# Kernel tuning notes

Measured on AMD Instinct MI355X. Metric: run time of the kernel, lower is better.

## Reference

```python
import jax, jax.numpy as jnp
import numpy as np

DIM = 1024
HEADS = 16
BLK = 129
DK = 64
DV = 64
B = 4
N = BLK * 32  # 4128


def setup_inputs() -> dict:
    key = jax.random.key(0)
    ks = jax.random.split(key, 6)
    inner_k = HEADS * DK
    inner_v = HEADS * DV
    s = 1.0 / np.sqrt(DIM)
    x = jax.random.normal(ks[0], (B, N, DIM), dtype=jnp.float32)
    Wq = jax.random.normal(ks[1], (inner_k, DIM), dtype=jnp.float32) * s
    Wk = jax.random.normal(ks[2], (inner_k, DIM), dtype=jnp.float32) * s
    Wv = jax.random.normal(ks[3], (inner_v, DIM), dtype=jnp.float32) * s
    Wo = jax.random.normal(ks[4], (DIM, inner_v), dtype=jnp.float32) * (1.0 / np.sqrt(inner_v))
    bo = jax.random.normal(ks[5], (DIM,), dtype=jnp.float32) * 0.01
    return {"x": x, "Wq": Wq, "Wk": Wk, "Wv": Wv, "Wo": Wo, "bo": bo}


def reference(x, Wq, Wk, Wv, Wo, bo):
    Bsz, Nlen, D = x.shape
    nb = Nlen // BLK
    scale = 1.0 / np.sqrt(DK)
    # projections (Linear without bias: x @ W.T)
    q = (x @ Wq.T).reshape(Bsz, nb, BLK, HEADS, DK)
    k = (x @ Wk.T).reshape(Bsz, nb, BLK, HEADS, DK)
    v = (x @ Wv.T).reshape(Bsz, nb, BLK, HEADS, DV)
    # block-local attention: each block attends within itself
    scores = jnp.einsum('bnqhd,bnkhd->bnhqk', q, k) * scale  # [B,nb,H,BLK,BLK]
    attn = jax.nn.softmax(scores, axis=-1)
    out_blk = jnp.einsum('bnhqk,bnkhd->bnhqd', attn, v)  # [B,nb,H,BLK,DV]
    # global attention among the first token of each block
    qg = q[:, :, 0]  # [B,nb,H,DK]
    kg = k[:, :, 0]
    vg = v[:, :, 0]
    sg = jnp.einsum('bqhd,bkhd->bhqk', qg, kg) * scale  # [B,H,nb,nb]
    ag = jax.nn.softmax(sg, axis=-1)
    out_g = jnp.einsum('bhqk,bkhd->bqhd', ag, vg)  # [B,nb,H,DV]
    # add global output onto position 0 of each block
    out_blk = out_blk.at[:, :, :, 0, :].add(out_g.transpose(0, 1, 2, 3).swapaxes(2, 2))  # out_g already [B,nb,H,DV]
    # reassemble to [B,N,H*DV]
    out = out_blk.transpose(0, 1, 3, 2, 4).reshape(Bsz, Nlen, HEADS * DV)
    return out @ Wo.T + bo
```

## Files before the change

### kernel.cpp

```cpp
#include <hip/hip_runtime.h>

typedef unsigned short u16;
typedef __attribute__((ext_vector_type(8))) __bf16 bf16x8;
typedef __attribute__((ext_vector_type(4))) float f32x4;
typedef __attribute__((ext_vector_type(8))) u16 u16x8;
typedef __attribute__((ext_vector_type(4))) u16 u16x4;

#define DIMSZ 1024
#define HEADS 16
#define BLKSZ 129
#define NBLK 32
#define NTOK (BLKSZ * NBLK)
#define BATCH 4
#define MROWS (BATCH * NTOK)

#define MFMA __builtin_amdgcn_mfma_f32_16x16x32_bf16

#define SSTR 152
#define KSTR 72

#define NKT 32

__device__ __forceinline__ float bf2f(u16 u) {
  return __uint_as_float(((unsigned)u) << 16);
}
__device__ __forceinline__ u16 f2bf(float f) {
  unsigned u = __float_as_uint(f);
  u += 0x7FFFu + ((u >> 16) & 1u);
  return (u16)(u >> 16);
}

#define GLD16(ldsp, gp) __builtin_amdgcn_global_load_lds( \
    (const __attribute__((address_space(1))) void*)(gp),   \
    (__attribute__((address_space(3))) void*)(ldsp), 16, 0, 0)

__global__ __launch_bounds__(256) void cast_f32_bf16(
    const float* __restrict__ in, u16* __restrict__ out, int n)
{
  int i = (blockIdx.x * 256 + threadIdx.x) * 4;
  if (i < n) {
    float4 f = *(const float4*)(in + i);
    u16x4 o = { f2bf(f.x), f2bf(f.y), f2bf(f.z), f2bf(f.w) };
    *(u16x4*)(out + i) = o;
  }
}

__device__ __forceinline__ int xcd_swz(int bid, int nwg) {
  const int xcd = bid & 7, l = bid >> 3;
  const int q = nwg >> 3, r = nwg & 7;
  return (xcd < r ? xcd * (q + 1) : r * (q + 1) + (xcd - r) * q) + l;
}

__device__ __forceinline__ void stage3(u16* slot, const u16* gA,
                                       const u16* gB, int tid) {
  GLD16(slot + tid * 8, gA);
  GLD16(slot + 4096 + tid * 8, gB);
  GLD16(slot + 8192 + tid * 8, gB + 128 * DIMSZ);
}

__device__ __forceinline__ void gemm_pipe(
    const u16* __restrict__ A, const u16* __restrict__ Bm,
    int m0, int n0, int tid, u16 (*sm)[12288], f32x4 (*acc)[4])
{
  const int lane = tid & 63, w = tid >> 6;
  const int qd = lane >> 4, l15 = lane & 15;
  const int wm = (w >> 2) * 64, wn = (w & 3) * 64;

  const u16* gA = A + (size_t)(m0 + (tid >> 2)) * DIMSZ + (tid & 3) * 8;
  const u16* gB = Bm + (size_t)(n0 + (tid >> 2)) * DIMSZ + (tid & 3) * 8;

  stage3(sm[0], gA, gB, tid);
  stage3(sm[1], gA + 32, gB + 32, tid);
  asm volatile("s_waitcnt vmcnt(3)" ::: "memory");
  __builtin_amdgcn_s_barrier();
  __builtin_amdgcn_sched_barrier(0);

#pragma unroll 4
  for (int t = 0; t < NKT; ++t) {
    if (t + 2 < NKT)
      stage3(sm[(t + 2) & 3], gA + (t + 2) * 32, gB + (t + 2) * 32, tid);

    const u16* slot = sm[t & 3];
    bf16x8 af[4], bv[4];
#pragma unroll
    for (int mi = 0; mi < 4; ++mi)
      af[mi] = *(const bf16x8*)&slot[(wm + mi * 16 + l15) * 32 + qd * 8];
#pragma unroll
    for (int ni = 0; ni < 4; ++ni)
      bv[ni] = *(const bf16x8*)&slot[4096 + (wn + ni * 16 + l15) * 32 + qd * 8];

    __builtin_amdgcn_s_setprio(1);
#pragma unroll
    for (int mi = 0; mi < 4; ++mi)
#pragma unroll
      for (int ni = 0; ni < 4; ++ni)
        acc[mi][ni] = MFMA(af[mi], bv[ni], acc[mi][ni], 0, 0, 0);
    __builtin_amdgcn_s_setprio(0);

    __builtin_amdgcn_sched_barrier(0);
    if (t + 2 < NKT) {
      asm volatile("s_waitcnt vmcnt(3)" ::: "memory");
    } else {
      asm volatile("s_waitcnt vmcnt(0)" ::: "memory");
    }
    __builtin_amdgcn_s_barrier();
    __builtin_amdgcn_sched_barrier(0);
  }
}

__global__ __launch_bounds__(512, 2) void gemm_qkv(
    const u16* __restrict__ A, const u16* __restrict__ B,
    u16* __restrict__ Cq, u16* __restrict__ Ck, u16* __restrict__ Cv)
{
  __shared__ u16 sm[4][12288];
  const int tid = threadIdx.x;
  f32x4 acc[4][4];
#pragma unroll
  for (int mi = 0; mi < 4; ++mi)
#pragma unroll
    for (int ni = 0; ni < 4; ++ni)
      acc[mi][ni] = (f32x4){0.f, 0.f, 0.f, 0.f};

  const int wg = xcd_swz(blockIdx.x, (MROWS / 128) * 12);
  const int nt = wg % 12, mt = wg / 12;
  const int m0 = mt * 128, n0 = nt * 256;

  gemm_pipe(A, B, m0, n0, tid, sm, acc);

  u16* C = nt < 4 ? Cq : (nt < 8 ? Ck : Cv);
  const int c0 = (nt & 3) * 256;
  const int lane = tid & 63, w = tid >> 6;
  const int qd = lane >> 4, l15 = lane & 15;
  const int wm = (w >> 2) * 64, wn = (w & 3) * 64;
#pragma unroll
  for (int mi = 0; mi < 4; ++mi)
#pragma unroll
    for (int ni = 0; ni < 4; ++ni) {
      const int row0 = m0 + wm + mi * 16 + qd * 4;
      const int col  = c0 + wn + ni * 16 + l15;
#pragma unroll
      for (int r = 0; r < 4; ++r)
        C[(size_t)(row0 + r) * DIMSZ + col] = f2bf(acc[mi][ni][r]);
    }
}

__global__ __launch_bounds__(512, 2) void gemm_out(
    const u16* __restrict__ A, const u16* __restrict__ B,
    float* __restrict__ C, const float* __restrict__ bias)
{
  __shared__ u16 sm[4][12288];
  const int tid = threadIdx.x;
  f32x4 acc[4][4];
#pragma unroll
  for (int mi = 0; mi < 4; ++mi)
#pragma unroll
    for (int ni = 0; ni < 4; ++ni)
      acc[mi][ni] = (f32x4){0.f, 0.f, 0.f, 0.f};

  const int wg = xcd_swz(blockIdx.x, (MROWS / 128) * 4);
  const int nt = wg % 4, mt = wg / 4;
  const int m0 = mt * 128, n0 = nt * 256;

  gemm_pipe(A, B, m0, n0, tid, sm, acc);

  const int lane = tid & 63, w = tid >> 6;
  const int qd = lane >> 4, l15 = lane & 15;
  const int wm = (w >> 2) * 64, wn = (w & 3) * 64;
#pragma unroll
  for (int mi = 0; mi < 4; ++mi)
#pragma unroll
    for (int ni = 0; ni < 4; ++ni) {
      const int row0 = m0 + wm + mi * 16 + qd * 4;
      const int col  = n0 + wn + ni * 16 + l15;
      float badd = bias[col];
#pragma unroll
      for (int r = 0; r < 4; ++r)
        C[(size_t)(row0 + r) * DIMSZ + col] = acc[mi][ni][r] + badd;
    }
}

__global__ __launch_bounds__(64) void global_attn(
    const u16* __restrict__ q, const u16* __restrict__ k,
    const u16* __restrict__ v, float* __restrict__ g)
{
  __shared__ float sQ[NBLK * 64];
  __shared__ float sKT[64 * NBLK];
  __shared__ float sV[NBLK * 64];
  __shared__ float sp[NBLK];
  const int b = blockIdx.x >> 4, h = blockIdx.x & 15;
  const int lane = threadIdx.x;

  for (int idx = lane; idx < NBLK * 64; idx += 64) {
    int j = idx >> 6, d = idx & 63;
    size_t off = ((size_t)(b * NTOK + j * BLKSZ)) * DIMSZ + h * 64 + d;
    sQ[idx] = bf2f(q[off]);
    sKT[d * NBLK + j] = bf2f(k[off]);
    sV[idx] = bf2f(v[off]);
  }
  __syncthreads();

  for (int i = 0; i < NBLK; ++i) {
    float s = -3.0e38f;
    if (lane < 32) {
      float acc = 0.f;
      for (int d = 0; d < 64; ++d) acc += sQ[i * 64 + d] * sKT[d * NBLK + lane];
      s = acc * 0.125f;
    }
    float m = s;
    for (int t = 1; t < 64; t <<= 1) m = fmaxf(m, __shfl_xor(m, t));
    float e = (lane < 32) ? __expf(s - m) : 0.f;
    float sum = e;
    for (int t = 1; t < 64; t <<= 1) sum += __shfl_xor(sum, t);
    if (lane < 32) sp[lane] = e / sum;
    __syncthreads();
    float acc = 0.f;
    for (int jj = 0; jj < NBLK; ++jj) acc += sp[jj] * sV[jj * 64 + lane];
    g[(((size_t)b * NBLK + i) * HEADS + h) * 64 + lane] = acc;
    __syncthreads();
  }
}

__global__ __launch_bounds__(512) void block_attn(
    const u16* q, const u16* __restrict__ k,
    const u16* __restrict__ v, const float* __restrict__ g,
    u16* ao)
{
  __shared__ u16 sS[144 * SSTR];
  __shared__ u16 sKV[144 * KSTR];
  const int b = blockIdx.x, blk = blockIdx.y, h = blockIdx.z;
  const int tid = threadIdx.x, lane = tid & 63, w = tid >> 6;
  const int qd = lane >> 4, l15 = lane & 15;
  const int h64 = h * 64;
  const size_t row_base = (size_t)b * NTOK + (size_t)blk * BLKSZ;
  const f32x4 zero4 = {0.f, 0.f, 0.f, 0.f};

  {
    const u16x8 zero8 = {0, 0, 0, 0, 0, 0, 0, 0};
    for (int c = tid; c < 144 * 8; c += 512) {
      int row = c >> 3, cc = c & 7;
      u16x8 val = zero8;
      if (row < BLKSZ)
        val = *(const u16x8*)(k + (row_base + row) * DIMSZ + h64 + cc * 8);
      *(u16x8*)&sKV[row * KSTR + cc * 8] = val;
    }
  }
  __syncthreads();

  for (int t = w; t < 81; t += 8) {
    int mt = t / 9, nt = t - mt * 9;
    int qrow = mt * 16 + l15;
    if (qrow > 128) qrow = 128;
    const u16* qp = q + (row_base + qrow) * DIMSZ + h64;
    bf16x8 qf0 = *(const bf16x8*)(qp + qd * 8);
    bf16x8 qf1 = *(const bf16x8*)(qp + 32 + qd * 8);
    bf16x8 kf0 = *(const bf16x8*)&sKV[(nt * 16 + l15) * KSTR + qd * 8];
    bf16x8 kf1 = *(const bf16x8*)&sKV[(nt * 16 + l15) * KSTR + 32 + qd * 8];
    f32x4 c = zero4;
    c = MFMA(qf0, kf0, c, 0, 0, 0);
    c = MFMA(qf1, kf1, c, 0, 0, 0);
    int r0 = mt * 16 + qd * 4, col = nt * 16 + l15;
#pragma unroll
    for (int r = 0; r < 4; ++r)
      sS[(r0 + r) * SSTR + col] = f2bf(c[r] * 0.125f);
  }
  __syncthreads();

  for (int c = tid; c < BLKSZ * 8; c += 512) {
    int row = c >> 3, cc = c & 7;
    u16x8 val = *(const u16x8*)(v + (row_base + row) * DIMSZ + h64 + cc * 8);
#pragma unroll
    for (int jj = 0; jj < 8; ++jj)
      sKV[(cc * 8 + jj) * SSTR + row] = val[jj];
  }

  for (int row = w; row < BLKSZ; row += 8) {
    float x1 = bf2f(sS[row * SSTR + lane]);
    float x2 = bf2f(sS[row * SSTR + 64 + lane]);
    float x3 = (lane == 0) ? bf2f(sS[row * SSTR + 128]) : -3.0e38f;
    float m = fmaxf(fmaxf(x1, x2), x3);
    for (int t = 1; t < 64; t <<= 1) m = fmaxf(m, __shfl_xor(m, t));
    float e1 = __expf(x1 - m), e2 = __expf(x2 - m);
    float e3 = (lane == 0) ? __expf(x3 - m) : 0.f;
    float s = e1 + e2 + e3;
    for (int t = 1; t < 64; t <<= 1) s += __shfl_xor(s, t);
    float inv = 1.f / s;
    sS[row * SSTR + lane] = f2bf(e1 * inv);
    sS[row * SSTR + 64 + lane] = f2bf(e2 * inv);
    if (lane == 0) sS[row * SSTR + 128] = f2bf(e3 * inv);
  }
  __syncthreads();

  for (int t = w; t < 36; t += 8) {
    int mt = t >> 2, nt = t & 3;
    f32x4 c = zero4;
#pragma unroll
    for (int kk = 0; kk < 128; kk += 32) {
      bf16x8 pf = *(const bf16x8*)&sS[(mt * 16 + l15) * SSTR + kk + qd * 8];
      bf16x8 vf = *(const bf16x8*)&sKV[(nt * 16 + l15) * SSTR + kk + qd * 8];
      c = MFMA(pf, vf, c, 0, 0, 0);
    }
    int dv = nt * 16 + l15;
    float v128 = bf2f(sKV[dv * SSTR + 128]);
    int r0 = mt * 16 + qd * 4;
#pragma unroll
    for (int r = 0; r < 4; ++r) {
      int row = r0 + r;
      if (row < BLKSZ) {
        float p128 = bf2f(sS[row * SSTR + 128]);
        float val = c[r] + p128 * v128;
        if (row == 0)
          val += g[(((size_t)b * NBLK + blk) * HEADS + h) * 64 + dv];
        ao[(row_base + row) * DIMSZ + h64 + dv] = f2bf(val);
      }
    }
  }
}

extern "C" void kernel_launch(void* const* d_in, const int* in_sizes, int n_in,
                              void* d_out, int out_size, void* d_ws, size_t ws_size,
                              hipStream_t stream) {
  const float* x  = (const float*)d_in[0];
  const float* Wq = (const float*)d_in[1];
  const float* Wk = (const float*)d_in[2];
  const float* Wv = (const float*)d_in[3];
  const float* Wo = (const float*)d_in[4];
  const float* bo = (const float*)d_in[5];
  float* out = (float*)d_out;

  char* ws = (char*)d_ws;
  const size_t xb = (size_t)MROWS * DIMSZ * sizeof(u16);
  float* gb     = (float*)ws;
  u16*   qb     = (u16*)(ws + (1u << 20));
  u16*   x16    = (u16*)(ws + (1u << 20) + xb);
  u16*   Wqkv16 = (u16*)(ws + (1u << 20) + 2 * xb);
  u16*   Wo16   = x16;
  u16*   kb     = (u16*)d_out;
  u16*   vb     = (u16*)d_out + (size_t)MROWS * DIMSZ;

  const int nx = MROWS * DIMSZ;
  const int nw = DIMSZ * DIMSZ;
  cast_f32_bf16<<<nx / 1024, 256, 0, stream>>>(x,  x16, nx);
  cast_f32_bf16<<<nw / 1024, 256, 0, stream>>>(Wq, Wqkv16,          nw);
  cast_f32_bf16<<<nw / 1024, 256, 0, stream>>>(Wk, Wqkv16 + nw,     nw);
  cast_f32_bf16<<<nw / 1024, 256, 0, stream>>>(Wv, Wqkv16 + 2 * nw, nw);

  gemm_qkv<<<dim3((MROWS / 128) * 12), 512, 0, stream>>>(x16, Wqkv16, qb, kb, vb);

  cast_f32_bf16<<<nw / 1024, 256, 0, stream>>>(Wo, Wo16, nw);

  global_attn<<<dim3(BATCH * HEADS), 64, 0, stream>>>(qb, kb, vb, gb);
  block_attn<<<dim3(BATCH, NBLK, HEADS), 512, 0, stream>>>(qb, kb, vb, gb, qb);
  gemm_out<<<dim3((MROWS / 128) * 4), 512, 0, stream>>>(qb, Wo16, out, bo);
}
```

Before: 464.1 us.

## Enlarge GEMM tiles to 256x256 and swizzle LDS chunks

```diff
diff --git a/kernel.cpp b/kernel.cpp
--- a/kernel.cpp
+++ b/kernel.cpp
@@ -51,47 +51,52 @@
   return (xcd < r ? xcd * (q + 1) : r * (q + 1) + (xcd - r) * q) + l;
 }
 
-__device__ __forceinline__ void stage3(u16* slot, const u16* gA,
-                                       const u16* gB, int tid) {
+__device__ __forceinline__ void stage_slot(u16* slot, const u16* gA,
+                                           const u16* gB, int tid) {
   GLD16(slot + tid * 8, gA);
-  GLD16(slot + 4096 + tid * 8, gB);
-  GLD16(slot + 8192 + tid * 8, gB + 128 * DIMSZ);
-}
-
-__device__ __forceinline__ void gemm_pipe(
+  GLD16(slot + 4096 + tid * 8, gA + 128 * DIMSZ);
+  GLD16(slot + 8192 + tid * 8, gB);
+  GLD16(slot + 12288 + tid * 8, gB + 128 * DIMSZ);
+}
+
+__device__ __forceinline__ void gemm_pipe256(
     const u16* __restrict__ A, const u16* __restrict__ Bm,
-    int m0, int n0, int tid, u16 (*sm)[12288], f32x4 (*acc)[4])
+    int m0, int n0, int tid, u16 (*sm)[16384], f32x4 (*acc)[4])
 {
   const int lane = tid & 63, w = tid >> 6;
   const int qd = lane >> 4, l15 = lane & 15;
-  const int wm = (w >> 2) * 64, wn = (w & 3) * 64;
-
-  const u16* gA = A + (size_t)(m0 + (tid >> 2)) * DIMSZ + (tid & 3) * 8;
-  const u16* gB = Bm + (size_t)(n0 + (tid >> 2)) * DIMSZ + (tid & 3) * 8;
-
-  stage3(sm[0], gA, gB, tid);
-  stage3(sm[1], gA + 32, gB + 32, tid);
-  asm volatile("s_waitcnt vmcnt(3)" ::: "memory");
+  const int wm = (w >> 2) * 128, wn = (w & 3) * 64;
+  const int qdsw = (qd ^ ((l15 >> 1) & 3)) * 8;
+
+  const int srow = tid >> 2;
+  const int schk = (tid & 3) ^ ((tid >> 3) & 3);
+  const u16* gA = A + (size_t)(m0 + srow) * DIMSZ + schk * 8;
+  const u16* gB = Bm + (size_t)(n0 + srow) * DIMSZ + schk * 8;
+
+  stage_slot(sm[0], gA, gB, tid);
+  stage_slot(sm[1], gA + 32, gB + 32, tid);
+  asm volatile("s_waitcnt vmcnt(4)" ::: "memory");
   __builtin_amdgcn_s_barrier();
   __builtin_amdgcn_sched_barrier(0);
 
 #pragma unroll 4
   for (int t = 0; t < NKT; ++t) {
     if (t + 2 < NKT)
-      stage3(sm[(t + 2) & 3], gA + (t + 2) * 32, gB + (t + 2) * 32, tid);
-
-    const u16* slot = sm[t & 3];
-    bf16x8 af[4], bv[4];
-#pragma unroll
-    for (int mi = 0; mi < 4; ++mi)
-      af[mi] = *(const bf16x8*)&slot[(wm + mi * 16 + l15) * 32 + qd * 8];
+      stage_slot(sm[(t + 2) & 3], gA + (t + 2) * 32, gB + (t + 2) * 32, tid);
+
+    const u16* sA = sm[t & 3];
+    const u16* sB = sm[t & 3] + 8192;
+    bf16x8 af[8], bv[4];
+#pragma unroll
+    for (int mi = 0; mi < 8; ++mi)
+      af[mi] = *(const bf16x8*)&sA[(wm + mi * 16 + l15) * 32 + qdsw];
 #pragma unroll
     for (int ni = 0; ni < 4; ++ni)
-      bv[ni] = *(const bf16x8*)&slot[4096 + (wn + ni * 16 + l15) * 32 + qd * 8];
+      bv[ni] = *(const bf16x8*)&sB[(wn + ni * 16 + l15) * 32 + qdsw];
 
     __builtin_amdgcn_s_setprio(1);
 #pragma unroll
-    for (int mi = 0; mi < 4; ++mi)
+    for (int mi = 0; mi < 8; ++mi)
 #pragma unroll
       for (int ni = 0; ni < 4; ++ni)
         acc[mi][ni] = MFMA(af[mi], bv[ni], acc[mi][ni], 0, 0, 0);
@@ -99,7 +104,7 @@
 
     __builtin_amdgcn_sched_barrier(0);
     if (t + 2 < NKT) {
-      asm volatile("s_waitcnt vmcnt(3)" ::: "memory");
+      asm volatile("s_waitcnt vmcnt(4)" ::: "memory");
     } else {
       asm volatile("s_waitcnt vmcnt(0)" ::: "memory");
     }
@@ -112,35 +117,36 @@
     const u16* __restrict__ A, const u16* __restrict__ B,
     u16* __restrict__ Cq, u16* __restrict__ Ck, u16* __restrict__ Cv)
 {
-  __shared__ u16 sm[4][12288];
+  __shared__ u16 sm[4][16384];
   const int tid = threadIdx.x;
-  f32x4 acc[4][4];
-#pragma unroll
-  for (int mi = 0; mi < 4; ++mi)
+  f32x4 acc[8][4];
+#pragma unroll
+  for (int mi = 0; mi < 8; ++mi)
 #pragma unroll
     for (int ni = 0; ni < 4; ++ni)
       acc[mi][ni] = (f32x4){0.f, 0.f, 0.f, 0.f};
 
-  const int wg = xcd_swz(blockIdx.x, (MROWS / 128) * 12);
+  const int wg = xcd_swz(blockIdx.x, 65 * 12);
   const int nt = wg % 12, mt = wg / 12;
-  const int m0 = mt * 128, n0 = nt * 256;
-
-  gemm_pipe(A, B, m0, n0, tid, sm, acc);
+  const int m0 = mt * 256, n0 = nt * 256;
+
+  gemm_pipe256(A, B, m0, n0, tid, sm, acc);
 
   u16* C = nt < 4 ? Cq : (nt < 8 ? Ck : Cv);
   const int c0 = (nt & 3) * 256;
   const int lane = tid & 63, w = tid >> 6;
   const int qd = lane >> 4, l15 = lane & 15;
-  const int wm = (w >> 2) * 64, wn = (w & 3) * 64;
-#pragma unroll
-  for (int mi = 0; mi < 4; ++mi)
+  const int wm = (w >> 2) * 128, wn = (w & 3) * 64;
+#pragma unroll
+  for (int mi = 0; mi < 8; ++mi)
 #pragma unroll
     for (int ni = 0; ni < 4; ++ni) {
       const int row0 = m0 + wm + mi * 16 + qd * 4;
       const int col  = c0 + wn + ni * 16 + l15;
 #pragma unroll
       for (int r = 0; r < 4; ++r)
-        C[(size_t)(row0 + r) * DIMSZ + col] = f2bf(acc[mi][ni][r]);
+        if (row0 + r < MROWS)
+          C[(size_t)(row0 + r) * DIMSZ + col] = f2bf(acc[mi][ni][r]);
     }
 }
 
@@ -148,26 +154,26 @@
     const u16* __restrict__ A, const u16* __restrict__ B,
     float* __restrict__ C, const float* __restrict__ bias)
 {
-  __shared__ u16 sm[4][12288];
+  __shared__ u16 sm[4][16384];
   const int tid = threadIdx.x;
-  f32x4 acc[4][4];
-#pragma unroll
-  for (int mi = 0; mi < 4; ++mi)
+  f32x4 acc[8][4];
+#pragma unroll
+  for (int mi = 0; mi < 8; ++mi)
 #pragma unroll
     for (int ni = 0; ni < 4; ++ni)
       acc[mi][ni] = (f32x4){0.f, 0.f, 0.f, 0.f};
 
-  const int wg = xcd_swz(blockIdx.x, (MROWS / 128) * 4);
+  const int wg = xcd_swz(blockIdx.x, 65 * 4);
   const int nt = wg % 4, mt = wg / 4;
-  const int m0 = mt * 128, n0 = nt * 256;
-
-  gemm_pipe(A, B, m0, n0, tid, sm, acc);
+  const int m0 = mt * 256, n0 = nt * 256;
+
+  gemm_pipe256(A, B, m0, n0, tid, sm, acc);
 
   const int lane = tid & 63, w = tid >> 6;
   const int qd = lane >> 4, l15 = lane & 15;
-  const int wm = (w >> 2) * 64, wn = (w & 3) * 64;
-#pragma unroll
-  for (int mi = 0; mi < 4; ++mi)
+  const int wm = (w >> 2) * 128, wn = (w & 3) * 64;
+#pragma unroll
+  for (int mi = 0; mi < 8; ++mi)
 #pragma unroll
     for (int ni = 0; ni < 4; ++ni) {
       const int row0 = m0 + wm + mi * 16 + qd * 4;
@@ -175,7 +181,8 @@
       float badd = bias[col];
 #pragma unroll
       for (int r = 0; r < 4; ++r)
-        C[(size_t)(row0 + r) * DIMSZ + col] = acc[mi][ni][r] + badd;
+        if (row0 + r < MROWS)
+          C[(size_t)(row0 + r) * DIMSZ + col] = acc[mi][ni][r] + badd;
     }
 }
 
@@ -344,11 +351,11 @@
   cast_f32_bf16<<<nw / 1024, 256, 0, stream>>>(Wk, Wqkv16 + nw,     nw);
   cast_f32_bf16<<<nw / 1024, 256, 0, stream>>>(Wv, Wqkv16 + 2 * nw, nw);
 
-  gemm_qkv<<<dim3((MROWS / 128) * 12), 512, 0, stream>>>(x16, Wqkv16, qb, kb, vb);
+  gemm_qkv<<<dim3(65 * 12), 512, 0, stream>>>(x16, Wqkv16, qb, kb, vb);
 
   cast_f32_bf16<<<nw / 1024, 256, 0, stream>>>(Wo, Wo16, nw);
 
   global_attn<<<dim3(BATCH * HEADS), 64, 0, stream>>>(qb, kb, vb, gb);
   block_attn<<<dim3(BATCH, NBLK, HEADS), 512, 0, stream>>>(qb, kb, vb, gb, qb);
-  gemm_out<<<dim3((MROWS / 128) * 4), 512, 0, stream>>>(qb, Wo16, out, bo);
-}
+  gemm_out<<<dim3(65 * 4), 512, 0, stream>>>(qb, Wo16, out, bo);
+}
```

Result: slower. 484.8 us (+4.5%).

## Switch GEMMs to 128x128 tiles with swizzled LDS and reuse Q fragments in block attention

Applied to the files above, without the earlier changes.

```diff
diff --git a/kernel.cpp b/kernel.cpp
--- a/kernel.cpp
+++ b/kernel.cpp
@@ -51,43 +51,47 @@
   return (xcd < r ? xcd * (q + 1) : r * (q + 1) + (xcd - r) * q) + l;
 }
 
-__device__ __forceinline__ void stage3(u16* slot, const u16* gA,
-                                       const u16* gB, int tid) {
+__device__ __forceinline__ void stage_sq(u16* slot, const u16* gA,
+                                         const u16* gB, int tid) {
   GLD16(slot + tid * 8, gA);
+  GLD16(slot + 2048 + tid * 8, gA + 64 * DIMSZ);
   GLD16(slot + 4096 + tid * 8, gB);
-  GLD16(slot + 8192 + tid * 8, gB + 128 * DIMSZ);
-}
-
-__device__ __forceinline__ void gemm_pipe(
+  GLD16(slot + 6144 + tid * 8, gB + 64 * DIMSZ);
+}
+
+__device__ __forceinline__ void gemm_pipe_sq(
     const u16* __restrict__ A, const u16* __restrict__ Bm,
-    int m0, int n0, int tid, u16 (*sm)[12288], f32x4 (*acc)[4])
+    int m0, int n0, int tid, u16 (*sm)[8192], f32x4 (*acc)[4])
 {
   const int lane = tid & 63, w = tid >> 6;
   const int qd = lane >> 4, l15 = lane & 15;
-  const int wm = (w >> 2) * 64, wn = (w & 3) * 64;
-
-  const u16* gA = A + (size_t)(m0 + (tid >> 2)) * DIMSZ + (tid & 3) * 8;
-  const u16* gB = Bm + (size_t)(n0 + (tid >> 2)) * DIMSZ + (tid & 3) * 8;
-
-  stage3(sm[0], gA, gB, tid);
-  stage3(sm[1], gA + 32, gB + 32, tid);
-  asm volatile("s_waitcnt vmcnt(3)" ::: "memory");
+  const int wm = (w >> 1) * 64, wn = (w & 1) * 64;
+  const int qdsw = (qd ^ ((l15 >> 1) & 3)) * 8;
+
+  const int srow = tid >> 2;
+  const int schk = (tid & 3) ^ ((tid >> 3) & 3);
+  const u16* gA = A + (size_t)(m0 + srow) * DIMSZ + schk * 8;
+  const u16* gB = Bm + (size_t)(n0 + srow) * DIMSZ + schk * 8;
+
+  stage_sq(sm[0], gA, gB, tid);
+  stage_sq(sm[1], gA + 32, gB + 32, tid);
+  asm volatile("s_waitcnt vmcnt(4)" ::: "memory");
   __builtin_amdgcn_s_barrier();
   __builtin_amdgcn_sched_barrier(0);
 
 #pragma unroll 4
   for (int t = 0; t < NKT; ++t) {
     if (t + 2 < NKT)
-      stage3(sm[(t + 2) & 3], gA + (t + 2) * 32, gB + (t + 2) * 32, tid);
+      stage_sq(sm[(t + 2) & 3], gA + (t + 2) * 32, gB + (t + 2) * 32, tid);
 
     const u16* slot = sm[t & 3];
     bf16x8 af[4], bv[4];
 #pragma unroll
     for (int mi = 0; mi < 4; ++mi)
-      af[mi] = *(const bf16x8*)&slot[(wm + mi * 16 + l15) * 32 + qd * 8];
+      af[mi] = *(const bf16x8*)&slot[(wm + mi * 16 + l15) * 32 + qdsw];
 #pragma unroll
     for (int ni = 0; ni < 4; ++ni)
-      bv[ni] = *(const bf16x8*)&slot[4096 + (wn + ni * 16 + l15) * 32 + qd * 8];
+      bv[ni] = *(const bf16x8*)&slot[4096 + (wn + ni * 16 + l15) * 32 + qdsw];
 
     __builtin_amdgcn_s_setprio(1);
 #pragma unroll
@@ -99,7 +103,7 @@
 
     __builtin_amdgcn_sched_barrier(0);
     if (t + 2 < NKT) {
-      asm volatile("s_waitcnt vmcnt(3)" ::: "memory");
+      asm volatile("s_waitcnt vmcnt(4)" ::: "memory");
     } else {
       asm volatile("s_waitcnt vmcnt(0)" ::: "memory");
     }
@@ -108,11 +112,11 @@
   }
 }
 
-__global__ __launch_bounds__(512, 2) void gemm_qkv(
+__global__ __launch_bounds__(256, 2) void gemm_qkv(
     const u16* __restrict__ A, const u16* __restrict__ B,
     u16* __restrict__ Cq, u16* __restrict__ Ck, u16* __restrict__ Cv)
 {
-  __shared__ u16 sm[4][12288];
+  __shared__ u16 sm[4][8192];
   const int tid = threadIdx.x;
   f32x4 acc[4][4];
 #pragma unroll
@@ -121,17 +125,17 @@
     for (int ni = 0; ni < 4; ++ni)
       acc[mi][ni] = (f32x4){0.f, 0.f, 0.f, 0.f};
 
-  const int wg = xcd_swz(blockIdx.x, (MROWS / 128) * 12);
-  const int nt = wg % 12, mt = wg / 12;
-  const int m0 = mt * 128, n0 = nt * 256;
-
-  gemm_pipe(A, B, m0, n0, tid, sm, acc);
-
-  u16* C = nt < 4 ? Cq : (nt < 8 ? Ck : Cv);
-  const int c0 = (nt & 3) * 256;
+  const int wg = xcd_swz(blockIdx.x, 129 * 24);
+  const int nt = wg % 24, mt = wg / 24;
+  const int m0 = mt * 128, n0 = nt * 128;
+
+  gemm_pipe_sq(A, B, m0, n0, tid, sm, acc);
+
+  u16* C = nt < 8 ? Cq : (nt < 16 ? Ck : Cv);
+  const int c0 = (nt & 7) * 128;
   const int lane = tid & 63, w = tid >> 6;
   const int qd = lane >> 4, l15 = lane & 15;
-  const int wm = (w >> 2) * 64, wn = (w & 3) * 64;
+  const int wm = (w >> 1) * 64, wn = (w & 1) * 64;
 #pragma unroll
   for (int mi = 0; mi < 4; ++mi)
 #pragma unroll
@@ -144,11 +148,11 @@
     }
 }
 
-__global__ __launch_bounds__(512, 2) void gemm_out(
+__global__ __launch_bounds__(256, 2) void gemm_out(
     const u16* __restrict__ A, const u16* __restrict__ B,
     float* __restrict__ C, const float* __restrict__ bias)
 {
-  __shared__ u16 sm[4][12288];
+  __shared__ u16 sm[4][8192];
   const int tid = threadIdx.x;
   f32x4 acc[4][4];
 #pragma unroll
@@ -157,15 +161,15 @@
     for (int ni = 0; ni < 4; ++ni)
       acc[mi][ni] = (f32x4){0.f, 0.f, 0.f, 0.f};
 
-  const int wg = xcd_swz(blockIdx.x, (MROWS / 128) * 4);
-  const int nt = wg % 4, mt = wg / 4;
-  const int m0 = mt * 128, n0 = nt * 256;
-
-  gemm_pipe(A, B, m0, n0, tid, sm, acc);
+  const int wg = xcd_swz(blockIdx.x, 129 * 8);
+  const int nt = wg & 7, mt = wg >> 3;
+  const int m0 = mt * 128, n0 = nt * 128;
+
+  gemm_pipe_sq(A, B, m0, n0, tid, sm, acc);
 
   const int lane = tid & 63, w = tid >> 6;
   const int qd = lane >> 4, l15 = lane & 15;
-  const int wm = (w >> 2) * 64, wn = (w & 3) * 64;
+  const int wm = (w >> 1) * 64, wn = (w & 1) * 64;
 #pragma unroll
   for (int mi = 0; mi < 4; ++mi)
 #pragma unroll
@@ -246,22 +250,31 @@
   }
   __syncthreads();
 
-  for (int t = w; t < 81; t += 8) {
-    int mt = t / 9, nt = t - mt * 9;
-    int qrow = mt * 16 + l15;
-    if (qrow > 128) qrow = 128;
-    const u16* qp = q + (row_base + qrow) * DIMSZ + h64;
-    bf16x8 qf0 = *(const bf16x8*)(qp + qd * 8);
-    bf16x8 qf1 = *(const bf16x8*)(qp + 32 + qd * 8);
-    bf16x8 kf0 = *(const bf16x8*)&sKV[(nt * 16 + l15) * KSTR + qd * 8];
-    bf16x8 kf1 = *(const bf16x8*)&sKV[(nt * 16 + l15) * KSTR + 32 + qd * 8];
-    f32x4 c = zero4;
-    c = MFMA(qf0, kf0, c, 0, 0, 0);
-    c = MFMA(qf1, kf1, c, 0, 0, 0);
-    int r0 = mt * 16 + qd * 4, col = nt * 16 + l15;
-#pragma unroll
-    for (int r = 0; r < 4; ++r)
-      sS[(r0 + r) * SSTR + col] = f2bf(c[r] * 0.125f);
+  {
+    const int tbeg = w * 10;
+    const int tend = (w == 7) ? 81 : tbeg + 10;
+    int cur_mt = -1;
+    bf16x8 qf0, qf1;
+    for (int t = tbeg; t < tend; ++t) {
+      int mt = t / 9, nt = t - mt * 9;
+      if (mt != cur_mt) {
+        cur_mt = mt;
+        int qrow = mt * 16 + l15;
+        if (qrow > 128) qrow = 128;
+        const u16* qp = q + (row_base + qrow) * DIMSZ + h64;
+        qf0 = *(const bf16x8*)(qp + qd * 8);
+        qf1 = *(const bf16x8*)(qp + 32 + qd * 8);
+      }
+      bf16x8 kf0 = *(const bf16x8*)&sKV[(nt * 16 + l15) * KSTR + qd * 8];
+      bf16x8 kf1 = *(const bf16x8*)&sKV[(nt * 16 + l15) * KSTR + 32 + qd * 8];
+      f32x4 c = zero4;
+      c = MFMA(qf0, kf0, c, 0, 0, 0);
+      c = MFMA(qf1, kf1, c, 0, 0, 0);
+      int r0 = mt * 16 + qd * 4, col = nt * 16 + l15;
+#pragma unroll
+      for (int r = 0; r < 4; ++r)
+        sS[(r0 + r) * SSTR + col] = f2bf(c[r] * 0.125f);
+    }
   }
   __syncthreads();
 
@@ -344,11 +357,11 @@
   cast_f32_bf16<<<nw / 1024, 256, 0, stream>>>(Wk, Wqkv16 + nw,     nw);
   cast_f32_bf16<<<nw / 1024, 256, 0, stream>>>(Wv, Wqkv16 + 2 * nw, nw);
 
-  gemm_qkv<<<dim3((MROWS / 128) * 12), 512, 0, stream>>>(x16, Wqkv16, qb, kb, vb);
+  gemm_qkv<<<dim3(129 * 24), 256, 0, stream>>>(x16, Wqkv16, qb, kb, vb);
 
   cast_f32_bf16<<<nw / 1024, 256, 0, stream>>>(Wo, Wo16, nw);
 
   global_attn<<<dim3(BATCH * HEADS), 64, 0, stream>>>(qb, kb, vb, gb);
   block_attn<<<dim3(BATCH, NBLK, HEADS), 512, 0, stream>>>(qb, kb, vb, gb, qb);
-  gemm_out<<<dim3((MROWS / 128) * 4), 512, 0, stream>>>(qb, Wo16, out, bo);
-}
+  gemm_out<<<dim3(129 * 8), 256, 0, stream>>>(qb, Wo16, out, bo);
+}
```

After: 432.5 us. 6.8% less time.
